# Kernel optimization log

Measured on AMD Instinct MI355X. Metric: run time of the kernel, lower is better.

The kernel has to match this reference:

```python
import jax, jax.numpy as jnp
import numpy as np
import math

D_SINGLE, D_PAIR, H, PQ, PV = 384, 128, 12, 4, 8
DH = D_SINGLE // H
OUT_DIM = H * DH + H * PV * 4 + H * D_PAIR


def setup_inputs() -> dict:
    key = jax.random.key(0)
    ks = jax.random.split(key, 24)
    B, L = 1, 512
    inp = {
        'single': jax.random.normal(ks[0], (B, L, D_SINGLE), jnp.float32),
        'pair': jax.random.normal(ks[1], (B, L, L, D_PAIR), jnp.float32),
        'rot_mats': jax.random.normal(ks[2], (B, L, 3, 3), jnp.float32),
        'trans': jax.random.normal(ks[3], (B, L, 3), jnp.float32),
        'mask': jnp.ones((B, L), jnp.float32),
        'ln_w': jnp.ones((D_SINGLE,), jnp.float32),
        'ln_b': jnp.zeros((D_SINGLE,), jnp.float32),
        'Wq': jax.random.normal(ks[4], (D_SINGLE, H * DH), jnp.float32) * 0.02,
        'bq': jnp.zeros((H * DH,), jnp.float32),
        'Wk': jax.random.normal(ks[5], (D_SINGLE, H * DH), jnp.float32) * 0.02,
        'bk': jnp.zeros((H * DH,), jnp.float32),
        'Wv': jax.random.normal(ks[6], (D_SINGLE, H * DH), jnp.float32) * 0.02,
        'bv': jnp.zeros((H * DH,), jnp.float32),
        'Wqp': jax.random.normal(ks[7], (D_SINGLE, H * PQ * 3), jnp.float32) * 0.02,
        'bqp': jnp.zeros((H * PQ * 3,), jnp.float32),
        'Wkp': jax.random.normal(ks[8], (D_SINGLE, H * PQ * 3), jnp.float32) * 0.02,
        'bkp': jnp.zeros((H * PQ * 3,), jnp.float32),
        'Wvp': jax.random.normal(ks[9], (D_SINGLE, H * PV * 3), jnp.float32) * 0.02,
        'bvp': jnp.zeros((H * PV * 3,), jnp.float32),
        'Wpb': jax.random.normal(ks[10], (D_PAIR, H), jnp.float32) * 0.02,
        'bpb': jnp.zeros((H,), jnp.float32),
        'Wo': jax.random.normal(ks[11], (OUT_DIM, D_SINGLE), jnp.float32) * 0.02,
        'bo': jnp.zeros((D_SINGLE,), jnp.float32),
        'w_c': jnp.asarray(1.0 / math.sqrt(3.0), jnp.float32),
        'w_l': jnp.asarray(1.0 / 3.0, jnp.float32),
        'gamma_h': jnp.ones((H,), jnp.float32),
    }
    return inp


def _layer_norm(x, w, b, eps=1e-5):
    mu = jnp.mean(x, axis=-1, keepdims=True)
    var = jnp.mean((x - mu) ** 2, axis=-1, keepdims=True)
    return (x - mu) * jax.lax.rsqrt(var + eps) * w + b


def reference(single, pair, rot_mats, trans, mask, ln_w, ln_b, Wq, bq, Wk, bk, Wv, bv,
              Wqp, bqp, Wkp, bkp, Wvp, bvp, Wpb, bpb, Wo, bo, w_c, w_l, gamma_h):
    B, L, _ = single.shape
    sn = _layer_norm(single, ln_w, ln_b)
    q = (sn @ Wq + bq).reshape(B, L, H, DH)
    k = (sn @ Wk + bk).reshape(B, L, H, DH)
    v = (sn @ Wv + bv).reshape(B, L, H, DH)
    qp = (sn @ Wqp + bqp).reshape(B, L, H, PQ, 3)
    kp = (sn @ Wkp + bkp).reshape(B, L, H, PQ, 3)
    vp = (sn @ Wvp + bvp).reshape(B, L, H, PV, 3)

    t = trans[:, :, None, None, :]  # [B,L,1,1,3]
    qg = jnp.einsum('blij,blhpj->blhpi', rot_mats, qp) + t
    kg = jnp.einsum('blij,blhpj->blhpi', rot_mats, kp) + t
    vg = jnp.einsum('blij,blhpj->blhpi', rot_mats, vp) + t

    # sequence logits [B,H,L,L]
    seq_logits = jnp.einsum('bihd,bjhd->bhij', q, k) * w_c / math.sqrt(DH)

    # geometric logits: pairwise point distances [B,H,L,L]
    q_pts = jnp.transpose(qg, (0, 2, 1, 3, 4))  # [B,H,L,PQ,3]
    k_pts = jnp.transpose(kg, (0, 2, 1, 3, 4))
    diff = q_pts[:, :, :, None] - k_pts[:, :, None]  # [B,H,L,L,PQ,3]
    dist_sq = jnp.sum(diff ** 2, axis=-1)            # [B,H,L,L,PQ]
    geo_logits = -0.5 * jnp.sum(dist_sq, axis=-1) * gamma_h[None, :, None, None] * w_l

    pair_bias = jnp.transpose(pair @ Wpb + bpb, (0, 3, 1, 2))  # [B,H,L,L]
    logits = seq_logits + geo_logits + pair_bias

    mask_2d = (mask[:, :, None] * mask[:, None, :])[:, None]  # [B,1,L,L]
    logits = jnp.where(mask_2d > 0, logits, jnp.float32(-1e9))
    attn = jax.nn.softmax(logits, axis=-1)  # [B,H,L,L]

    # sequence aggregation -> [B,L,H,DH]
    seq_out = jnp.einsum('bhij,bjhd->bihd', attn, v).reshape(B, L, H * DH)

    # point aggregation -> local frame features
    pts_out = jnp.einsum('bhij,bjhpd->bihpd', attn, vg)  # [B,L,H,PV,3]
    pts_local = jnp.einsum('blji,blhpj->blhpi', rot_mats, pts_out - t)
    pts_norm = jnp.linalg.norm(pts_local, axis=-1, keepdims=True)
    pts_feat = jnp.concatenate([pts_norm, pts_local], axis=-1).reshape(B, L, H * PV * 4)

    # pair aggregation -> [B,L,H*D_PAIR]
    pair_out = jnp.einsum('bhij,bijd->bihd', attn, pair).reshape(B, L, H * D_PAIR)

    combined = jnp.concatenate([seq_out, pts_feat, pair_out], axis=-1)
    return combined @ Wo + bo
```

## Files before the change

### kernel.cpp

```cpp
#include <hip/hip_runtime.h>
#include <math.h>

#define LQ    512
#define DS    384
#define DPAIR 128
#define NH    12
#define NPP   1792
#define TJC   64
#define NC    8

typedef unsigned short u16;
typedef unsigned int   u32;
typedef __attribute__((ext_vector_type(8))) short bf16x8;
typedef __attribute__((ext_vector_type(4))) float f32x4;

__device__ inline u16 bf16_rne(float x) {
  u32 u = __float_as_uint(x);
  u32 r = (u + 0x7FFFu + ((u >> 16) & 1u)) >> 16;
  return (u16)r;
}
__device__ inline void split_bf16(float x, u16& h, u16& l) {
  u16 hb = bf16_rne(x);
  float hf = __uint_as_float(((u32)hb) << 16);
  h = hb;
  l = bf16_rne(x - hf);
}

__global__ __launch_bounds__(256) void k_prep(
    const float* __restrict__ Wq, const float* __restrict__ Wk,
    const float* __restrict__ Wv, const float* __restrict__ Wqp,
    const float* __restrict__ Wkp, const float* __restrict__ Wvp,
    const float* __restrict__ bq, const float* __restrict__ bk,
    const float* __restrict__ bv, const float* __restrict__ bqp,
    const float* __restrict__ bkp, const float* __restrict__ bvp,
    const float* __restrict__ Wpb, const float* __restrict__ Wo,
    const float* __restrict__ xs, const float* __restrict__ ln_w,
    const float* __restrict__ ln_b,
    u16* __restrict__ Wth, u16* __restrict__ Wtl,
    float* __restrict__ bcat, float* __restrict__ WpbT,
    u16* __restrict__ WoTh, u16* __restrict__ WoTl,
    u16* __restrict__ snh, u16* __restrict__ snl) {
  __shared__ u16 sh_hi[64][66], sh_lo[64][66];
  int blk = blockIdx.x, t = threadIdx.x;
  if (blk < 168) {
    int kb = blk / 28, cb = blk % 28;
    int k0 = kb * 64, c0 = cb * 64;
    for (int e = t; e < 4096; e += 256) {
      int rr = e >> 6, cc = e & 63;
      int k = k0 + rr, c = c0 + cc;
      float v = 0.f;
      if (c < 384)       v = Wq[k*384 + c];
      else if (c < 768)  v = Wk[k*384 + c-384];
      else if (c < 1152) v = Wv[k*384 + c-768];
      else if (c < 1296) v = Wqp[k*144 + c-1152];
      else if (c < 1440) v = Wkp[k*144 + c-1296];
      else if (c < 1728) v = Wvp[k*288 + c-1440];
      u16 h_, l_; split_bf16(v, h_, l_);
      sh_hi[rr][cc] = h_; sh_lo[rr][cc] = l_;
    }
    __syncthreads();
    for (int e = t; e < 4096; e += 256) {
      int cc = e >> 6, kk = e & 63;
      Wth[(size_t)(c0+cc)*DS + k0 + kk] = sh_hi[kk][cc];
      Wtl[(size_t)(c0+cc)*DS + k0 + kk] = sh_lo[kk][cc];
    }
  } else if (blk == 168) {
    for (int e = t; e < NPP + NH*DPAIR; e += 256) {
      if (e < NPP) {
        int c = e;
        float v = 0.f;
        if (c < 384)       v = bq[c];
        else if (c < 768)  v = bk[c-384];
        else if (c < 1152) v = bv[c-768];
        else if (c < 1296) v = bqp[c-1152];
        else if (c < 1440) v = bkp[c-1296];
        else if (c < 1728) v = bvp[c-1440];
        bcat[c] = v;
      } else {
        int e2 = e - NPP;
        int k = e2 / NH, h = e2 % NH;
        WpbT[h*DPAIR + k] = Wpb[e2];
      }
    }
  } else if (blk < 385) {
    int idx = blk - 169;
    int kt = idx % 36, nt = idx / 36;
    int k0 = kt * 64, n0 = nt * 64;
    for (int e = t; e < 4096; e += 256) {
      int rr = e >> 6, cc = e & 63;
      float v = Wo[(size_t)(k0+rr)*384 + n0 + cc];
      u16 h_, l_; split_bf16(v, h_, l_);
      sh_hi[rr][cc] = h_; sh_lo[rr][cc] = l_;
    }
    __syncthreads();
    for (int e = t; e < 4096; e += 256) {
      int cc = e >> 6, kk = e & 63;
      WoTh[(size_t)(n0+cc)*2304 + k0 + kk] = sh_hi[kk][cc];
      WoTl[(size_t)(n0+cc)*2304 + k0 + kk] = sh_lo[kk][cc];
    }
  } else {
    int i = blk - 385;
    float* red = (float*)&sh_hi[0][0];
    float a0 = xs[i*DS + t];
    float a1 = (t < 128) ? xs[i*DS + 256 + t] : 0.f;
    red[t] = a0 + a1; __syncthreads();
    for (int s = 128; s > 0; s >>= 1) { if (t < s) red[t] += red[t+s]; __syncthreads(); }
    float mu = red[0] * (1.f/384.f);
    __syncthreads();
    float d0 = a0 - mu, d1 = (t < 128) ? (a1 - mu) : 0.f;
    red[t] = d0*d0 + d1*d1; __syncthreads();
    for (int s = 128; s > 0; s >>= 1) { if (t < s) red[t] += red[t+s]; __syncthreads(); }
    float rstd = rsqrtf(red[0] * (1.f/384.f) + 1e-5f);
    u16 h_, l_;
    float y0 = d0*rstd*ln_w[t] + ln_b[t];
    split_bf16(y0, h_, l_); snh[i*DS + t] = h_; snl[i*DS + t] = l_;
    if (t < 128) {
      float y1 = d1*rstd*ln_w[256+t] + ln_b[256+t];
      split_bf16(y1, h_, l_); snh[i*DS + 256 + t] = h_; snl[i*DS + 256 + t] = l_;
    }
  }
}

__global__ __launch_bounds__(256) void k_gemm_mfma(
    const u16* __restrict__ Ah, const u16* __restrict__ Al,
    const u16* __restrict__ Bth, const u16* __restrict__ Btl,
    const float* __restrict__ bias, float* __restrict__ C,
    float* __restrict__ Cpart, int M, int N, int K) {
  int t = threadIdx.x;
  int lane = t & 63, wave = t >> 6;
  int wr = wave >> 1, wc = wave & 1;
  int i0 = blockIdx.y * 64 + wr * 32;
  int j0 = blockIdx.x * 64 + wc * 32;
  int KS = gridDim.z;
  int kper = K / KS;
  size_t kbeg = (size_t)blockIdx.z * kper;
  int lr = lane & 15, lk = (lane >> 4) << 3;

  const u16* a0h = Ah  + (size_t)(i0 + lr) * K + kbeg + lk;
  const u16* a1h = a0h + (size_t)16 * K;
  const u16* a0l = Al  + (size_t)(i0 + lr) * K + kbeg + lk;
  const u16* a1l = a0l + (size_t)16 * K;
  const u16* b0h = Bth + (size_t)(j0 + lr) * K + kbeg + lk;
  const u16* b1h = b0h + (size_t)16 * K;
  const u16* b0l = Btl + (size_t)(j0 + lr) * K + kbeg + lk;
  const u16* b1l = b0l + (size_t)16 * K;

  f32x4 c00 = {0.f,0.f,0.f,0.f}, c01 = c00, c10 = c00, c11 = c00;
  for (int k = 0; k < kper; k += 32) {
    bf16x8 A0h = *(const bf16x8*)(a0h + k);
    bf16x8 A1h = *(const bf16x8*)(a1h + k);
    bf16x8 B0h = *(const bf16x8*)(b0h + k);
    bf16x8 B1h = *(const bf16x8*)(b1h + k);
    bf16x8 A0l = *(const bf16x8*)(a0l + k);
    bf16x8 A1l = *(const bf16x8*)(a1l + k);
    bf16x8 B0l = *(const bf16x8*)(b0l + k);
    bf16x8 B1l = *(const bf16x8*)(b1l + k);
    c00 = __builtin_amdgcn_mfma_f32_16x16x32_bf16(A0h, B0h, c00, 0, 0, 0);
    c01 = __builtin_amdgcn_mfma_f32_16x16x32_bf16(A0h, B1h, c01, 0, 0, 0);
    c10 = __builtin_amdgcn_mfma_f32_16x16x32_bf16(A1h, B0h, c10, 0, 0, 0);
    c11 = __builtin_amdgcn_mfma_f32_16x16x32_bf16(A1h, B1h, c11, 0, 0, 0);
    c00 = __builtin_amdgcn_mfma_f32_16x16x32_bf16(A0h, B0l, c00, 0, 0, 0);
    c01 = __builtin_amdgcn_mfma_f32_16x16x32_bf16(A0h, B1l, c01, 0, 0, 0);
    c10 = __builtin_amdgcn_mfma_f32_16x16x32_bf16(A1h, B0l, c10, 0, 0, 0);
    c11 = __builtin_amdgcn_mfma_f32_16x16x32_bf16(A1h, B1l, c11, 0, 0, 0);
    c00 = __builtin_amdgcn_mfma_f32_16x16x32_bf16(A0l, B0h, c00, 0, 0, 0);
    c01 = __builtin_amdgcn_mfma_f32_16x16x32_bf16(A0l, B1h, c01, 0, 0, 0);
    c10 = __builtin_amdgcn_mfma_f32_16x16x32_bf16(A1l, B0h, c10, 0, 0, 0);
    c11 = __builtin_amdgcn_mfma_f32_16x16x32_bf16(A1l, B1h, c11, 0, 0, 0);
  }

  int orow = (lane >> 4) << 2;
  int col0 = j0 + lr, col1 = j0 + 16 + lr;
  if (KS == 1) {
    float bb0 = bias[col0], bb1 = bias[col1];
    #pragma unroll
    for (int r = 0; r < 4; r++) {
      int row0 = i0 + orow + r, row1 = row0 + 16;
      C[(size_t)row0*N + col0] = c00[r] + bb0;
      C[(size_t)row0*N + col1] = c01[r] + bb1;
      C[(size_t)row1*N + col0] = c10[r] + bb0;
      C[(size_t)row1*N + col1] = c11[r] + bb1;
    }
  } else {
    float* dst = Cpart + (size_t)blockIdx.z * M * N;
    #pragma unroll
    for (int r = 0; r < 4; r++) {
      int row0 = i0 + orow + r, row1 = row0 + 16;
      dst[(size_t)row0*N + col0] = c00[r];
      dst[(size_t)row0*N + col1] = c01[r];
      dst[(size_t)row1*N + col0] = c10[r];
      dst[(size_t)row1*N + col1] = c11[r];
    }
  }
}

__global__ void k_reduce_bias(const float* __restrict__ part, const float* __restrict__ bias,
                              float* __restrict__ out, int MN, int N, int KS) {
  int e = blockIdx.x * 256 + threadIdx.x;
  if (e >= MN) return;
  float s = bias[e % N];
  for (int z = 0; z < KS; z++) s += part[(size_t)z*MN + e];
  out[e] = s;
}

__global__ __launch_bounds__(256) void k_feat_logits(
    const float* __restrict__ C1, const float* __restrict__ rot,
    const float* __restrict__ trans, const float* __restrict__ gamma,
    const float* __restrict__ w_c, const float* __restrict__ w_l,
    float* __restrict__ S) {
  __shared__ u16 Ash[64][72], Asl[64][72], Bsh[64][72], Bsl[64][72];
  int h = blockIdx.z;
  int i0 = blockIdx.y * 64, j0 = blockIdx.x * 64;
  int t = threadIdx.x;

  if (t < 128) {
    int row = t & 63, side = t >> 6;
    int gi = (side ? j0 : i0) + row;
    float R[9], tr[3];
    #pragma unroll
    for (int r = 0; r < 9; r++) R[r] = rot[(size_t)gi*9 + r];
    #pragma unroll
    for (int r = 0; r < 3; r++) tr[r] = trans[(size_t)gi*3 + r];
    float sc = w_c[0] * rsqrtf(32.f);
    float gp = gamma[h] * w_l[0];
    u16 (*Fh)[72] = side ? Bsh : Ash;
    u16 (*Fl)[72] = side ? Bsl : Asl;
    const float* qk = C1 + (size_t)gi*NPP + (side ? 384 : 0) + h*32;
    u16 h_, l_;
    #pragma unroll 8
    for (int d = 0; d < 32; d++) {
      float v = side ? qk[d] : sc*qk[d];
      split_bf16(v, h_, l_); Fh[row][d] = h_; Fl[row][d] = l_;
    }
    const float* pp = C1 + (size_t)gi*NPP + (side ? 1296 : 1152) + h*12;
    float ss = 0.f;
    #pragma unroll
    for (int p = 0; p < 4; p++) {
      float x = pp[p*3], y = pp[p*3+1], z = pp[p*3+2];
      #pragma unroll
      for (int r = 0; r < 3; r++) {
        float g = fmaf(R[r*3],x, fmaf(R[r*3+1],y, fmaf(R[r*3+2],z, tr[r])));
        float v = side ? g : gp*g;
        split_bf16(v, h_, l_); Fh[row][32+p*3+r] = h_; Fl[row][32+p*3+r] = l_;
        ss = fmaf(g,g,ss);
      }
    }
    float c44 = side ? 1.f : -0.5f*gp*ss;
    float c45 = side ? -0.5f*gp*ss : 1.f;
    split_bf16(c44, h_, l_); Fh[row][44] = h_; Fl[row][44] = l_;
    split_bf16(c45, h_, l_); Fh[row][45] = h_; Fl[row][45] = l_;
    #pragma unroll
    for (int d = 46; d < 64; d++) { Fh[row][d] = 0; Fl[row][d] = 0; }
  }
  __syncthreads();

  int lane = t & 63, wave = t >> 6, wr = wave >> 1, wc = wave & 1;
  int lr = lane & 15, lk = (lane >> 4) << 3;
  f32x4 c00 = {0.f,0.f,0.f,0.f}, c01 = c00, c10 = c00, c11 = c00;
  #pragma unroll
  for (int ks = 0; ks < 64; ks += 32) {
    bf16x8 A0h = *(const bf16x8*)&Ash[wr*32 + lr][ks + lk];
    bf16x8 A1h = *(const bf16x8*)&Ash[wr*32 + 16 + lr][ks + lk];
    bf16x8 B0h = *(const bf16x8*)&Bsh[wc*32 + lr][ks + lk];
    bf16x8 B1h = *(const bf16x8*)&Bsh[wc*32 + 16 + lr][ks + lk];
    bf16x8 A0l = *(const bf16x8*)&Asl[wr*32 + lr][ks + lk];
    bf16x8 A1l = *(const bf16x8*)&Asl[wr*32 + 16 + lr][ks + lk];
    bf16x8 B0l = *(const bf16x8*)&Bsl[wc*32 + lr][ks + lk];
    bf16x8 B1l = *(const bf16x8*)&Bsl[wc*32 + 16 + lr][ks + lk];
    c00 = __builtin_amdgcn_mfma_f32_16x16x32_bf16(A0h, B0h, c00, 0, 0, 0);
    c01 = __builtin_amdgcn_mfma_f32_16x16x32_bf16(A0h, B1h, c01, 0, 0, 0);
    c10 = __builtin_amdgcn_mfma_f32_16x16x32_bf16(A1h, B0h, c10, 0, 0, 0);
    c11 = __builtin_amdgcn_mfma_f32_16x16x32_bf16(A1h, B1h, c11, 0, 0, 0);
    c00 = __builtin_amdgcn_mfma_f32_16x16x32_bf16(A0h, B0l, c00, 0, 0, 0);
    c01 = __builtin_amdgcn_mfma_f32_16x16x32_bf16(A0h, B1l, c01, 0, 0, 0);
    c10 = __builtin_amdgcn_mfma_f32_16x16x32_bf16(A1h, B0l, c10, 0, 0, 0);
    c11 = __builtin_amdgcn_mfma_f32_16x16x32_bf16(A1h, B1l, c11, 0, 0, 0);
    c00 = __builtin_amdgcn_mfma_f32_16x16x32_bf16(A0l, B0h, c00, 0, 0, 0);
    c01 = __builtin_amdgcn_mfma_f32_16x16x32_bf16(A0l, B1h, c01, 0, 0, 0);
    c10 = __builtin_amdgcn_mfma_f32_16x16x32_bf16(A1l, B0h, c10, 0, 0, 0);
    c11 = __builtin_amdgcn_mfma_f32_16x16x32_bf16(A1l, B1h, c11, 0, 0, 0);
  }

  int orow = (lane >> 4) << 2;
  int col0 = j0 + wc*32 + lr, col1 = col0 + 16;
  int rbase = i0 + wr*32 + orow;
  #pragma unroll
  for (int r = 0; r < 4; r++) {
    S[((size_t)h*LQ + rbase + r)*LQ + col0]      = c00[r];
    S[((size_t)h*LQ + rbase + r)*LQ + col1]      = c01[r];
    S[((size_t)h*LQ + rbase + 16 + r)*LQ + col0] = c10[r];
    S[((size_t)h*LQ + rbase + 16 + r)*LQ + col1] = c11[r];
  }
}

__global__ __launch_bounds__(256) void k_vt(
    const float* __restrict__ C1, const float* __restrict__ rot,
    const float* __restrict__ trans,
    u16* __restrict__ Vth, u16* __restrict__ Vtl) {
  int h = blockIdx.x;
  int i = blockIdx.y * 256 + threadIdx.x;
  float R[9], tr[3];
  #pragma unroll
  for (int r = 0; r < 9; r++) R[r] = rot[(size_t)i*9 + r];
  #pragma unroll
  for (int r = 0; r < 3; r++) tr[r] = trans[(size_t)i*3 + r];
  const float* vrow = C1 + (size_t)i*NPP + 768 + h*32;
  const float* prow = C1 + (size_t)i*NPP + 1440 + h*24;
  u16 h_, l_;
  #pragma unroll 8
  for (int n = 0; n < 32; n++) {
    split_bf16(vrow[n], h_, l_);
    Vth[((size_t)h*64 + n)*LQ + i] = h_;
    Vtl[((size_t)h*64 + n)*LQ + i] = l_;
  }
  #pragma unroll
  for (int p = 0; p < 8; p++) {
    float x = prow[p*3], y = prow[p*3+1], z = prow[p*3+2];
    #pragma unroll
    for (int r = 0; r < 3; r++) {
      float g = fmaf(R[r*3],x, fmaf(R[r*3+1],y, fmaf(R[r*3+2],z, tr[r])));
      split_bf16(g, h_, l_);
      Vth[((size_t)h*64 + 32 + p*3 + r)*LQ + i] = h_;
      Vtl[((size_t)h*64 + 32 + p*3 + r)*LQ + i] = l_;
    }
  }
  #pragma unroll
  for (int n = 56; n < 64; n++) {
    Vth[((size_t)h*64 + n)*LQ + i] = 0;
    Vtl[((size_t)h*64 + n)*LQ + i] = 0;
  }
}

__global__ __launch_bounds__(256, 2) void k_pair_chunk(
    const float* __restrict__ pair, const float* __restrict__ WpbT,
    const float* __restrict__ bpb, const float* __restrict__ mask,
    float* __restrict__ S, float* __restrict__ pairpart, float* __restrict__ msum) {
  __shared__ float tile[TJC*133];
  __shared__ float wt[NH*TJC];
  int i = blockIdx.x, c = blockIdx.y, t = threadIdx.x;
  int j0 = c*TJC;

  const float4* src = (const float4*)(pair + ((size_t)i*LQ + j0)*DPAIR);
  #pragma unroll
  for (int u = 0; u < 8; u++) {
    int e = t + u*256; int row = e >> 5, c4 = e & 31;
    *(float4*)&tile[row*133 + c4*4] = src[e];
  }

  int j = t & 63;
  int hg = __builtin_amdgcn_readfirstlane(t >> 6);
  int h0 = hg*3;
  float l[3];
  #pragma unroll
  for (int q = 0; q < 3; q++)
    l[q] = S[((size_t)(h0+q)*LQ + i)*LQ + j0 + j] + bpb[h0+q];
  bool dead = (mask[i] * mask[j0 + j] <= 0.f);
  __syncthreads();

  {
    const float* w0p = WpbT + (size_t)(h0+0)*DPAIR;
    const float* w1p = WpbT + (size_t)(h0+1)*DPAIR;
    const float* w2p = WpbT + (size_t)(h0+2)*DPAIR;
    float a0 = 0.f, a1 = 0.f, a2 = 0.f;
    #pragma unroll 8
    for (int k = 0; k < DPAIR; k += 4) {
      float4 pv = *(const float4*)&tile[j*133 + k];
      float4 w0 = *(const float4*)(w0p + k);
      float4 w1 = *(const float4*)(w1p + k);
      float4 w2 = *(const float4*)(w2p + k);
      a0 = fmaf(pv.x,w0.x, fmaf(pv.y,w0.y, fmaf(pv.z,w0.z, fmaf(pv.w,w0.w, a0))));
      a1 = fmaf(pv.x,w1.x, fmaf(pv.y,w1.y, fmaf(pv.z,w1.z, fmaf(pv.w,w1.w, a1))));
      a2 = fmaf(pv.x,w2.x, fmaf(pv.y,w2.y, fmaf(pv.z,w2.z, fmaf(pv.w,w2.w, a2))));
    }
    l[0] += a0; l[1] += a1; l[2] += a2;
    if (dead) { l[0] = -1e9f; l[1] = -1e9f; l[2] = -1e9f; }
  }

  #pragma unroll
  for (int q = 0; q < 3; q++) {
    float m = l[q];
    #pragma unroll
    for (int o = 32; o > 0; o >>= 1) m = fmaxf(m, __shfl_xor(m, o, 64));
    float w = __expf(l[q] - m);
    float sm = w;
    #pragma unroll
    for (int o = 32; o > 0; o >>= 1) sm += __shfl_xor(sm, o, 64);
    wt[(h0+q)*TJC + j] = w;
    S[((size_t)(h0+q)*LQ + i)*LQ + j0 + j] = w;
    if (j == 0) {
      float* dst = msum + (((size_t)i*NC + c)*NH + h0 + q)*2;
      dst[0] = m; dst[1] = sm;
    }
  }
  __syncthreads();

  int dg = t & 31, strip = t >> 5, jb = strip*8;
  float4 pv[8];
  #pragma unroll
  for (int q = 0; q < 8; q++) pv[q] = *(const float4*)&tile[(jb+q)*133 + dg*4];
  float4 acc[NH];
  #pragma unroll
  for (int h = 0; h < NH; h++) acc[h] = make_float4(0.f,0.f,0.f,0.f);
  #pragma unroll
  for (int h = 0; h < NH; h++) {
    float4 w0 = *(const float4*)&wt[h*TJC + jb];
    float4 w1 = *(const float4*)&wt[h*TJC + jb + 4];
    float wq[8] = {w0.x,w0.y,w0.z,w0.w,w1.x,w1.y,w1.z,w1.w};
    float4 a = acc[h];
    #pragma unroll
    for (int q = 0; q < 8; q++) {
      a.x = fmaf(wq[q], pv[q].x, a.x);
      a.y = fmaf(wq[q], pv[q].y, a.y);
      a.z = fmaf(wq[q], pv[q].z, a.z);
      a.w = fmaf(wq[q], pv[q].w, a.w);
    }
    acc[h] = a;
  }
  __syncthreads();

  float4* red4 = (float4*)tile;
  float4 tot[2];
  tot[0] = make_float4(0.f,0.f,0.f,0.f);
  tot[1] = make_float4(0.f,0.f,0.f,0.f);
  #pragma unroll
  for (int half = 0; half < 2; half++) {
    if ((strip >> 2) == half) {
      #pragma unroll
      for (int h = 0; h < NH; h++)
        red4[(((strip & 3)*NH) + h)*32 + dg] = acc[h];
    }
    __syncthreads();
    for (int e = t, u = 0; e < NH*32; e += 256, u++) {
      int rh = e >> 5, rd = e & 31;
      #pragma unroll
      for (int s4 = 0; s4 < 4; s4++) {
        float4 v = red4[((s4*NH) + rh)*32 + rd];
        tot[u].x += v.x; tot[u].y += v.y; tot[u].z += v.z; tot[u].w += v.w;
      }
    }
    __syncthreads();
  }
  for (int e = t, u = 0; e < NH*32; e += 256, u++) {
    int rh = e >> 5, rd = e & 31;
    *(float4*)&pairpart[(((size_t)i*NC + c)*NH + rh)*DPAIR + rd*4] = tot[u];
  }
}

__global__ __launch_bounds__(384) void k_scs_pairout(
    const float* __restrict__ msum, const float* __restrict__ pairpart,
    float* __restrict__ scs_g,
    u16* __restrict__ combh, u16* __restrict__ combl) {
  __shared__ float scs[NH*NC];
  int i = blockIdx.x, t = threadIdx.x;
  if (t < NH) {
    float m = -3.0e38f;
    float mc[NC], sc_[NC];
    #pragma unroll
    for (int c = 0; c < NC; c++) {
      const float* p = msum + (((size_t)i*NC + c)*NH + t)*2;
      mc[c] = p[0]; sc_[c] = p[1];
      m = fmaxf(m, mc[c]);
    }
    float s = 0.f;
    #pragma unroll
    for (int c = 0; c < NC; c++) s += sc_[c] * __expf(mc[c] - m);
    float inv = 1.f / s;
    #pragma unroll
    for (int c = 0; c < NC; c++) {
      float v = __expf(mc[c] - m) * inv;
      scs[t*NC + c] = v;
      scs_g[((size_t)i*NH + t)*NC + c] = v;
    }
  }
  __syncthreads();
  int h = t >> 5, d = t & 31;
  float4 tot = make_float4(0.f,0.f,0.f,0.f);
  #pragma unroll
  for (int c = 0; c < NC; c++) {
    float sc = scs[h*NC + c];
    float4 v = *(const float4*)&pairpart[(((size_t)i*NC + c)*NH + h)*DPAIR + d*4];
    tot.x = fmaf(v.x, sc, tot.x); tot.y = fmaf(v.y, sc, tot.y);
    tot.z = fmaf(v.z, sc, tot.z); tot.w = fmaf(v.w, sc, tot.w);
  }
  size_t dst = (size_t)i*2304 + 768 + h*DPAIR + d*4;
  u16 h_, l_;
  split_bf16(tot.x, h_, l_); combh[dst+0] = h_; combl[dst+0] = l_;
  split_bf16(tot.y, h_, l_); combh[dst+1] = h_; combl[dst+1] = l_;
  split_bf16(tot.z, h_, l_); combh[dst+2] = h_; combl[dst+2] = l_;
  split_bf16(tot.w, h_, l_); combh[dst+3] = h_; combl[dst+3] = l_;
}

__global__ __launch_bounds__(256) void k_attn_mfma(
    const float* __restrict__ S, const float* __restrict__ scs_g,
    const u16* __restrict__ Vth, const u16* __restrict__ Vtl,
    float* __restrict__ psum) {
  int t = threadIdx.x;
  int lane = t & 63, wave = t >> 6;
  int wr = wave >> 1, wc = wave & 1;
  int z = blockIdx.x;
  int i0 = blockIdx.y * 64 + wr * 32;
  int h = blockIdx.z;
  int n0 = wc * 32;
  int lr = lane & 15, lk = (lane >> 4) << 3;

  const float* a0p = S + ((size_t)h*LQ + i0 + lr)*LQ + z*128 + lk;
  const float* a1p = a0p + (size_t)16*LQ;
  const float* s0p = scs_g + ((size_t)(i0 + lr)*NH + h)*NC + z*2;
  const float* s1p = scs_g + ((size_t)(i0 + 16 + lr)*NH + h)*NC + z*2;
  const u16* b0h = Vth + ((size_t)h*64 + n0 + lr)*LQ + z*128 + lk;
  const u16* b1h = b0h + (size_t)16*LQ;
  const u16* b0l = Vtl + ((size_t)h*64 + n0 + lr)*LQ + z*128 + lk;
  const u16* b1l = b0l + (size_t)16*LQ;

  f32x4 c00 = {0.f,0.f,0.f,0.f}, c01 = c00, c10 = c00, c11 = c00;
  #pragma unroll
  for (int k = 0; k < 128; k += 32) {
    int cc = (k >= 64) ? 1 : 0;
    float sc0 = s0p[cc], sc1 = s1p[cc];
    float4 av00 = *(const float4*)(a0p + k);
    float4 av01 = *(const float4*)(a0p + k + 4);
    float4 av10 = *(const float4*)(a1p + k);
    float4 av11 = *(const float4*)(a1p + k + 4);
    float a0v[8] = {av00.x,av00.y,av00.z,av00.w,av01.x,av01.y,av01.z,av01.w};
    float a1v[8] = {av10.x,av10.y,av10.z,av10.w,av11.x,av11.y,av11.z,av11.w};
    bf16x8 A0h = {}, A0l = {}, A1h = {}, A1l = {};
    #pragma unroll
    for (int e = 0; e < 8; e++) {
      u16 hh, ll;
      split_bf16(a0v[e]*sc0, hh, ll);
      A0h[e] = (short)hh; A0l[e] = (short)ll;
      split_bf16(a1v[e]*sc1, hh, ll);
      A1h[e] = (short)hh; A1l[e] = (short)ll;
    }
    bf16x8 B0h = *(const bf16x8*)(b0h + k);
    bf16x8 B1h = *(const bf16x8*)(b1h + k);
    bf16x8 B0l = *(const bf16x8*)(b0l + k);
    bf16x8 B1l = *(const bf16x8*)(b1l + k);
    c00 = __builtin_amdgcn_mfma_f32_16x16x32_bf16(A0h, B0h, c00, 0, 0, 0);
    c01 = __builtin_amdgcn_mfma_f32_16x16x32_bf16(A0h, B1h, c01, 0, 0, 0);
    c10 = __builtin_amdgcn_mfma_f32_16x16x32_bf16(A1h, B0h, c10, 0, 0, 0);
    c11 = __builtin_amdgcn_mfma_f32_16x16x32_bf16(A1h, B1h, c11, 0, 0, 0);
    c00 = __builtin_amdgcn_mfma_f32_16x16x32_bf16(A0h, B0l, c00, 0, 0, 0);
    c01 = __builtin_amdgcn_mfma_f32_16x16x32_bf16(A0h, B1l, c01, 0, 0, 0);
    c10 = __builtin_amdgcn_mfma_f32_16x16x32_bf16(A1h, B0l, c10, 0, 0, 0);
    c11 = __builtin_amdgcn_mfma_f32_16x16x32_bf16(A1h, B1l, c11, 0, 0, 0);
    c00 = __builtin_amdgcn_mfma_f32_16x16x32_bf16(A0l, B0h, c00, 0, 0, 0);
    c01 = __builtin_amdgcn_mfma_f32_16x16x32_bf16(A0l, B1h, c01, 0, 0, 0);
    c10 = __builtin_amdgcn_mfma_f32_16x16x32_bf16(A1l, B0h, c10, 0, 0, 0);
    c11 = __builtin_amdgcn_mfma_f32_16x16x32_bf16(A1l, B1h, c11, 0, 0, 0);
  }

  int orow = (lane >> 4) << 2;
  int col0 = n0 + lr, col1 = n0 + 16 + lr;
  #pragma unroll
  for (int r = 0; r < 4; r++) {
    int row0 = i0 + orow + r, row1 = row0 + 16;
    psum[(((size_t)z*LQ + row0)*NH + h)*64 + col0] = c00[r];
    psum[(((size_t)z*LQ + row0)*NH + h)*64 + col1] = c01[r];
    psum[(((size_t)z*LQ + row1)*NH + h)*64 + col0] = c10[r];
    psum[(((size_t)z*LQ + row1)*NH + h)*64 + col1] = c11[r];
  }
}

__global__ void k_avpts(const float* __restrict__ psum, const float* __restrict__ rot,
                        const float* __restrict__ trans,
                        u16* __restrict__ combh, u16* __restrict__ combl) {
  int idx = blockIdx.x * 256 + threadIdx.x;
  if (idx >= LQ*NH*40) return;
  int w = idx % 40; int ih = idx / 40; int h = ih % NH; int i = ih / NH;
  size_t base = ((size_t)i*NH + h)*64;
  u16 h_, l_;
  if (w < 32) {
    float s = 0.f;
    for (int z = 0; z < 4; z++) s += psum[(size_t)z*LQ*NH*64 + base + w];
    split_bf16(s, h_, l_);
    combh[(size_t)i*2304 + h*32 + w] = h_;
    combl[(size_t)i*2304 + h*32 + w] = l_;
  } else {
    int p = w - 32;
    float g[3];
    #pragma unroll
    for (int r = 0; r < 3; r++) {
      int n = 32 + p*3 + r;
      float s = 0.f;
      for (int z = 0; z < 4; z++) s += psum[(size_t)z*LQ*NH*64 + base + n];
      g[r] = s;
    }
    const float* R = rot + (size_t)i*9;
    const float* tr = trans + (size_t)i*3;
    float x = g[0]-tr[0], y = g[1]-tr[1], z = g[2]-tr[2];
    float lx = fmaf(R[0],x, fmaf(R[3],y, R[6]*z));
    float ly = fmaf(R[1],x, fmaf(R[4],y, R[7]*z));
    float lz = fmaf(R[2],x, fmaf(R[5],y, R[8]*z));
    float nrm = sqrtf(fmaf(lx,lx, fmaf(ly,ly, lz*lz)));
    size_t dst = (size_t)i*2304 + 384 + (h*8 + p)*4;
    split_bf16(nrm, h_, l_); combh[dst+0] = h_; combl[dst+0] = l_;
    split_bf16(lx,  h_, l_); combh[dst+1] = h_; combl[dst+1] = l_;
    split_bf16(ly,  h_, l_); combh[dst+2] = h_; combl[dst+2] = l_;
    split_bf16(lz,  h_, l_); combh[dst+3] = h_; combl[dst+3] = l_;
  }
}

extern "C" void kernel_launch(void* const* d_in, const int* in_sizes, int n_in,
                              void* d_out, int out_size, void* d_ws, size_t ws_size,
                              hipStream_t stream) {
  const float* single = (const float*)d_in[0];
  const float* pair   = (const float*)d_in[1];
  const float* rot    = (const float*)d_in[2];
  const float* trans  = (const float*)d_in[3];
  const float* mask   = (const float*)d_in[4];
  const float* ln_w   = (const float*)d_in[5];
  const float* ln_b   = (const float*)d_in[6];
  const float* Wq     = (const float*)d_in[7];
  const float* bq     = (const float*)d_in[8];
  const float* Wk     = (const float*)d_in[9];
  const float* bk     = (const float*)d_in[10];
  const float* Wv     = (const float*)d_in[11];
  const float* bv     = (const float*)d_in[12];
  const float* Wqp    = (const float*)d_in[13];
  const float* bqp    = (const float*)d_in[14];
  const float* Wkp    = (const float*)d_in[15];
  const float* bkp    = (const float*)d_in[16];
  const float* Wvp    = (const float*)d_in[17];
  const float* bvp    = (const float*)d_in[18];
  const float* Wpb    = (const float*)d_in[19];
  const float* bpb    = (const float*)d_in[20];
  const float* Wo     = (const float*)d_in[21];
  const float* bo     = (const float*)d_in[22];
  const float* w_c    = (const float*)d_in[23];
  const float* w_l    = (const float*)d_in[24];
  const float* gamma  = (const float*)d_in[25];
  float* out = (float*)d_out;

  float* p = (float*)d_ws;
  auto alloc = [&](size_t n) { float* r = p; p += n; return r; };
  u16* WcatTh = (u16*)alloc((size_t)NPP*DS/2);
  u16* WcatTl = (u16*)alloc((size_t)NPP*DS/2);
  u16* snh    = (u16*)alloc((size_t)LQ*DS/2);
  u16* snl    = (u16*)alloc((size_t)LQ*DS/2);
  u16* WoTh   = (u16*)alloc((size_t)DS*2304/2);
  u16* WoTl   = (u16*)alloc((size_t)DS*2304/2);
  u16* combh  = (u16*)alloc((size_t)LQ*2304/2);
  u16* combl  = (u16*)alloc((size_t)LQ*2304/2);
  u16* Vth    = (u16*)alloc((size_t)NH*64*LQ/2);
  u16* Vtl    = (u16*)alloc((size_t)NH*64*LQ/2);
  float* bcat    = alloc(NPP);
  float* WpbT    = alloc((size_t)NH*DPAIR);
  float* C1      = alloc((size_t)LQ*NPP);
  float* S       = alloc((size_t)NH*LQ*LQ);
  float* pairpart= alloc((size_t)LQ*NC*NH*DPAIR);
  float* msum    = alloc((size_t)LQ*NC*NH*2);
  float* scs_g   = alloc((size_t)LQ*NH*NC);
  float* psum    = alloc((size_t)4*LQ*NH*64);
  float* outpart = alloc((size_t)8*LQ*DS);

  k_prep<<<dim3(897), 256, 0, stream>>>(
      Wq, Wk, Wv, Wqp, Wkp, Wvp, bq, bk, bv, bqp, bkp, bvp, Wpb, Wo,
      single, ln_w, ln_b, WcatTh, WcatTl, bcat, WpbT, WoTh, WoTl, snh, snl);
  k_gemm_mfma<<<dim3(NPP/64, LQ/64, 1), 256, 0, stream>>>(
      snh, snl, WcatTh, WcatTl, bcat, C1, nullptr, LQ, NPP, DS);
  k_feat_logits<<<dim3(LQ/64, LQ/64, NH), 256, 0, stream>>>(
      C1, rot, trans, gamma, w_c, w_l, S);
  k_vt<<<dim3(NH, LQ/256), 256, 0, stream>>>(C1, rot, trans, Vth, Vtl);
  k_pair_chunk<<<dim3(LQ, NC), 256, 0, stream>>>(
      pair, WpbT, bpb, mask, S, pairpart, msum);
  k_scs_pairout<<<dim3(LQ), 384, 0, stream>>>(
      msum, pairpart, scs_g, combh, combl);
  k_attn_mfma<<<dim3(4, LQ/64, NH), 256, 0, stream>>>(
      S, scs_g, Vth, Vtl, psum);
  k_avpts<<<dim3((LQ*NH*40 + 255)/256), 256, 0, stream>>>(
      psum, rot, trans, combh, combl);
  k_gemm_mfma<<<dim3(DS/64, LQ/64, 8), 256, 0, stream>>>(
      combh, combl, WoTh, WoTl, nullptr, nullptr, outpart, LQ, DS, 2304);
  k_reduce_bias<<<dim3((LQ*DS + 255)/256), 256, 0, stream>>>(outpart, bo, out, LQ*DS, DS, 8);
}
```

Before: 347.2 us.

## Store pair tile as bf16 in LDS and pre-split attention weights

k_pair_chunk now rounds the pair tile to bf16 in shared memory, roughly halving LDS use so four blocks can fit per CU instead of two. The pair-bias and pair-aggregation inputs lose precision, which changes results against the fp32 reference. The chunk-softmax rescale and hi/lo bf16 split of the attention weights move from k_attn_mfma into k_scs_pairout, which writes two bf16 weight arrays that the MFMA kernel loads directly. This removes per-element split work inside the attention kernel but adds an extra full pass over S and new global writes.

```diff
diff --git a/kernel.cpp b/kernel.cpp
--- a/kernel.cpp
+++ b/kernel.cpp
@@ -8,6 +8,7 @@
 #define NPP   1792
 #define TJC   64
 #define NC    8
+#define TSTR  140
 
 typedef unsigned short u16;
 typedef unsigned int   u32;
@@ -24,6 +25,9 @@
   float hf = __uint_as_float(((u32)hb) << 16);
   h = hb;
   l = bf16_rne(x - hf);
+}
+__device__ inline float bf16_to_f32(u16 b) {
+  return __uint_as_float(((u32)b) << 16);
 }
 
 __global__ __launch_bounds__(256) void k_prep(
@@ -331,12 +335,15 @@
   }
 }
 
-__global__ __launch_bounds__(256, 2) void k_pair_chunk(
+__global__ __launch_bounds__(256, 4) void k_pair_chunk(
     const float* __restrict__ pair, const float* __restrict__ WpbT,
     const float* __restrict__ bpb, const float* __restrict__ mask,
     float* __restrict__ S, float* __restrict__ pairpart, float* __restrict__ msum) {
-  __shared__ float tile[TJC*133];
-  __shared__ float wt[NH*TJC];
+  __shared__ __align__(16) char lds_raw[24576];
+  u16*   tile = (u16*)lds_raw;
+  float* wt   = (float*)(lds_raw + 64*TSTR*2);
+  float4* red4 = (float4*)lds_raw;
+
   int i = blockIdx.x, c = blockIdx.y, t = threadIdx.x;
   int j0 = c*TJC;
 
@@ -344,7 +351,11 @@
   #pragma unroll
   for (int u = 0; u < 8; u++) {
     int e = t + u*256; int row = e >> 5, c4 = e & 31;
-    *(float4*)&tile[row*133 + c4*4] = src[e];
+    float4 v = src[e];
+    ushort4 b;
+    b.x = bf16_rne(v.x); b.y = bf16_rne(v.y);
+    b.z = bf16_rne(v.z); b.w = bf16_rne(v.w);
+    *(ushort4*)&tile[row*TSTR + c4*4] = b;
   }
 
   int j = t & 63;
@@ -364,13 +375,15 @@
     float a0 = 0.f, a1 = 0.f, a2 = 0.f;
     #pragma unroll 8
     for (int k = 0; k < DPAIR; k += 4) {
-      float4 pv = *(const float4*)&tile[j*133 + k];
+      ushort4 pb = *(const ushort4*)&tile[j*TSTR + k];
+      float px = bf16_to_f32(pb.x), py = bf16_to_f32(pb.y);
+      float pz = bf16_to_f32(pb.z), pw = bf16_to_f32(pb.w);
       float4 w0 = *(const float4*)(w0p + k);
       float4 w1 = *(const float4*)(w1p + k);
       float4 w2 = *(const float4*)(w2p + k);
-      a0 = fmaf(pv.x,w0.x, fmaf(pv.y,w0.y, fmaf(pv.z,w0.z, fmaf(pv.w,w0.w, a0))));
-      a1 = fmaf(pv.x,w1.x, fmaf(pv.y,w1.y, fmaf(pv.z,w1.z, fmaf(pv.w,w1.w, a1))));
-      a2 = fmaf(pv.x,w2.x, fmaf(pv.y,w2.y, fmaf(pv.z,w2.z, fmaf(pv.w,w2.w, a2))));
+      a0 = fmaf(px,w0.x, fmaf(py,w0.y, fmaf(pz,w0.z, fmaf(pw,w0.w, a0))));
+      a1 = fmaf(px,w1.x, fmaf(py,w1.y, fmaf(pz,w1.z, fmaf(pw,w1.w, a1))));
+      a2 = fmaf(px,w2.x, fmaf(py,w2.y, fmaf(pz,w2.z, fmaf(pw,w2.w, a2))));
     }
     l[0] += a0; l[1] += a1; l[2] += a2;
     if (dead) { l[0] = -1e9f; l[1] = -1e9f; l[2] = -1e9f; }
@@ -397,7 +410,11 @@
   int dg = t & 31, strip = t >> 5, jb = strip*8;
   float4 pv[8];
   #pragma unroll
-  for (int q = 0; q < 8; q++) pv[q] = *(const float4*)&tile[(jb+q)*133 + dg*4];
+  for (int q = 0; q < 8; q++) {
+    ushort4 pb = *(const ushort4*)&tile[(jb+q)*TSTR + dg*4];
+    pv[q].x = bf16_to_f32(pb.x); pv[q].y = bf16_to_f32(pb.y);
+    pv[q].z = bf16_to_f32(pb.z); pv[q].w = bf16_to_f32(pb.w);
+  }
   float4 acc[NH];
   #pragma unroll
   for (int h = 0; h < NH; h++) acc[h] = make_float4(0.f,0.f,0.f,0.f);
@@ -418,7 +435,6 @@
   }
   __syncthreads();
 
-  float4* red4 = (float4*)tile;
   float4 tot[2];
   tot[0] = make_float4(0.f,0.f,0.f,0.f);
   tot[1] = make_float4(0.f,0.f,0.f,0.f);
@@ -448,7 +464,8 @@
 
 __global__ __launch_bounds__(384) void k_scs_pairout(
     const float* __restrict__ msum, const float* __restrict__ pairpart,
-    float* __restrict__ scs_g,
+    const float* __restrict__ S,
+    u16* __restrict__ Awh, u16* __restrict__ Awl,
     u16* __restrict__ combh, u16* __restrict__ combl) {
   __shared__ float scs[NH*NC];
   int i = blockIdx.x, t = threadIdx.x;
@@ -466,11 +483,8 @@
     for (int c = 0; c < NC; c++) s += sc_[c] * __expf(mc[c] - m);
     float inv = 1.f / s;
     #pragma unroll
-    for (int c = 0; c < NC; c++) {
-      float v = __expf(mc[c] - m) * inv;
-      scs[t*NC + c] = v;
-      scs_g[((size_t)i*NH + t)*NC + c] = v;
-    }
+    for (int c = 0; c < NC; c++)
+      scs[t*NC + c] = __expf(mc[c] - m) * inv;
   }
   __syncthreads();
   int h = t >> 5, d = t & 31;
@@ -482,16 +496,23 @@
     tot.x = fmaf(v.x, sc, tot.x); tot.y = fmaf(v.y, sc, tot.y);
     tot.z = fmaf(v.z, sc, tot.z); tot.w = fmaf(v.w, sc, tot.w);
   }
-  size_t dst = (size_t)i*2304 + 768 + h*DPAIR + d*4;
+  size_t cb = (size_t)i*2304 + 768 + h*DPAIR + d*4;
   u16 h_, l_;
-  split_bf16(tot.x, h_, l_); combh[dst+0] = h_; combl[dst+0] = l_;
-  split_bf16(tot.y, h_, l_); combh[dst+1] = h_; combl[dst+1] = l_;
-  split_bf16(tot.z, h_, l_); combh[dst+2] = h_; combl[dst+2] = l_;
-  split_bf16(tot.w, h_, l_); combh[dst+3] = h_; combl[dst+3] = l_;
+  split_bf16(tot.x, h_, l_); combh[cb+0] = h_; combl[cb+0] = l_;
+  split_bf16(tot.y, h_, l_); combh[cb+1] = h_; combl[cb+1] = l_;
+  split_bf16(tot.z, h_, l_); combh[cb+2] = h_; combl[cb+2] = l_;
+  split_bf16(tot.w, h_, l_); combh[cb+3] = h_; combl[cb+3] = l_;
+  for (int e = t; e < NH*LQ; e += 384) {
+    int hh2 = e >> 9, j = e & 511;
+    float w = S[((size_t)hh2*LQ + i)*LQ + j] * scs[hh2*NC + (j >> 6)];
+    split_bf16(w, h_, l_);
+    Awh[((size_t)hh2*LQ + i)*LQ + j] = h_;
+    Awl[((size_t)hh2*LQ + i)*LQ + j] = l_;
+  }
 }
 
 __global__ __launch_bounds__(256) void k_attn_mfma(
-    const float* __restrict__ S, const float* __restrict__ scs_g,
+    const u16* __restrict__ Awh, const u16* __restrict__ Awl,
     const u16* __restrict__ Vth, const u16* __restrict__ Vtl,
     float* __restrict__ psum) {
   int t = threadIdx.x;
@@ -502,38 +523,26 @@
   int h = blockIdx.z;
   int n0 = wc * 32;
   int lr = lane & 15, lk = (lane >> 4) << 3;
-
-  const float* a0p = S + ((size_t)h*LQ + i0 + lr)*LQ + z*128 + lk;
-  const float* a1p = a0p + (size_t)16*LQ;
-  const float* s0p = scs_g + ((size_t)(i0 + lr)*NH + h)*NC + z*2;
-  const float* s1p = scs_g + ((size_t)(i0 + 16 + lr)*NH + h)*NC + z*2;
-  const u16* b0h = Vth + ((size_t)h*64 + n0 + lr)*LQ + z*128 + lk;
+  size_t kb = (size_t)z*128 + lk;
+
+  const u16* a0h = Awh + ((size_t)h*LQ + i0 + lr)*LQ + kb;
+  const u16* a1h = a0h + (size_t)16*LQ;
+  const u16* a0l = Awl + ((size_t)h*LQ + i0 + lr)*LQ + kb;
+  const u16* a1l = a0l + (size_t)16*LQ;
+  const u16* b0h = Vth + ((size_t)h*64 + n0 + lr)*LQ + kb;
   const u16* b1h = b0h + (size_t)16*LQ;
-  const u16* b0l = Vtl + ((size_t)h*64 + n0 + lr)*LQ + z*128 + lk;
+  const u16* b0l = Vtl + ((size_t)h*64 + n0 + lr)*LQ + kb;
   const u16* b1l = b0l + (size_t)16*LQ;
 
   f32x4 c00 = {0.f,0.f,0.f,0.f}, c01 = c00, c10 = c00, c11 = c00;
   #pragma unroll
   for (int k = 0; k < 128; k += 32) {
-    int cc = (k >= 64) ? 1 : 0;
-    float sc0 = s0p[cc], sc1 = s1p[cc];
-    float4 av00 = *(const float4*)(a0p + k);
-    float4 av01 = *(const float4*)(a0p + k + 4);
-    float4 av10 = *(const float4*)(a1p + k);
-    float4 av11 = *(const float4*)(a1p + k + 4);
-    float a0v[8] = {av00.x,av00.y,av00.z,av00.w,av01.x,av01.y,av01.z,av01.w};
-    float a1v[8] = {av10.x,av10.y,av10.z,av10.w,av11.x,av11.y,av11.z,av11.w};
-    bf16x8 A0h = {}, A0l = {}, A1h = {}, A1l = {};
-    #pragma unroll
-    for (int e = 0; e < 8; e++) {
-      u16 hh, ll;
-      split_bf16(a0v[e]*sc0, hh, ll);
-      A0h[e] = (short)hh; A0l[e] = (short)ll;
-      split_bf16(a1v[e]*sc1, hh, ll);
-      A1h[e] = (short)hh; A1l[e] = (short)ll;
-    }
+    bf16x8 A0h = *(const bf16x8*)(a0h + k);
+    bf16x8 A1h = *(const bf16x8*)(a1h + k);
     bf16x8 B0h = *(const bf16x8*)(b0h + k);
     bf16x8 B1h = *(const bf16x8*)(b1h + k);
+    bf16x8 A0l = *(const bf16x8*)(a0l + k);
+    bf16x8 A1l = *(const bf16x8*)(a1l + k);
     bf16x8 B0l = *(const bf16x8*)(b0l + k);
     bf16x8 B1l = *(const bf16x8*)(b1l + k);
     c00 = __builtin_amdgcn_mfma_f32_16x16x32_bf16(A0h, B0h, c00, 0, 0, 0);
@@ -644,13 +653,14 @@
   u16* combl  = (u16*)alloc((size_t)LQ*2304/2);
   u16* Vth    = (u16*)alloc((size_t)NH*64*LQ/2);
   u16* Vtl    = (u16*)alloc((size_t)NH*64*LQ/2);
+  u16* Awh    = (u16*)alloc((size_t)NH*LQ*LQ/2);
+  u16* Awl    = (u16*)alloc((size_t)NH*LQ*LQ/2);
   float* bcat    = alloc(NPP);
   float* WpbT    = alloc((size_t)NH*DPAIR);
   float* C1      = alloc((size_t)LQ*NPP);
   float* S       = alloc((size_t)NH*LQ*LQ);
   float* pairpart= alloc((size_t)LQ*NC*NH*DPAIR);
   float* msum    = alloc((size_t)LQ*NC*NH*2);
-  float* scs_g   = alloc((size_t)LQ*NH*NC);
   float* psum    = alloc((size_t)4*LQ*NH*64);
   float* outpart = alloc((size_t)8*LQ*DS);
 
@@ -665,9 +675,9 @@
   k_pair_chunk<<<dim3(LQ, NC), 256, 0, stream>>>(
       pair, WpbT, bpb, mask, S, pairpart, msum);
   k_scs_pairout<<<dim3(LQ), 384, 0, stream>>>(
-      msum, pairpart, scs_g, combh, combl);
+      msum, pairpart, S, Awh, Awl, combh, combl);
   k_attn_mfma<<<dim3(4, LQ/64, NH), 256, 0, stream>>>(
-      S, scs_g, Vth, Vtl, psum);
+      Awh, Awl, Vth, Vtl, psum);
   k_avpts<<<dim3((LQ*NH*40 + 255)/256), 256, 0, stream>>>(
       psum, rot, trans, combh, combl);
   k_gemm_mfma<<<dim3(DS/64, LQ/64, 8), 256, 0, stream>>>(
```

Result: no change. 345.3 us (-0.5%).
